# Optimization experiments

Measured on AMD Instinct MI355X. Metric: run time of the kernel, lower is better.

## Reference

```python
import jax, jax.numpy as jnp
import numpy as np


def _cdist(x, y):
    # x: (b, n, c), y: (b, m, c) -> (b, n, m) Euclidean distances
    x2 = jnp.sum(x * x, axis=-1, keepdims=True)          # (b, n, 1)
    y2 = jnp.sum(y * y, axis=-1)[:, None, :]             # (b, 1, m)
    xy = jnp.einsum('bnc,bmc->bnm', x, y)                # (b, n, m)
    d2 = jnp.maximum(x2 + y2 - 2.0 * xy, 0.0)
    return jnp.sqrt(d2)


def setup_inputs() -> dict:
    key = jax.random.key(0)
    k1, k2, k3, k4 = jax.random.split(key, 4)
    bs, N, M, C = 8, 4096, 4096, 128
    return {
        'set1': jax.random.normal(k1, (bs, N, C), dtype=jnp.float32),
        'set2': jax.random.normal(k2, (bs, M, C), dtype=jnp.float32),
        'w1': jax.random.uniform(k3, (bs, N), dtype=jnp.float32),
        'w2': jax.random.uniform(k4, (bs, M), dtype=jnp.float32),
    }


def reference(set1, set2, w1, w2):
    dist = _cdist(set1, set2)                 # (b, N, M)
    out_dist = jnp.min(dist, axis=2)          # (b, N)
    out_dist2 = jnp.min(dist, axis=1)         # (b, M)
    total = (jnp.sum(w1 * out_dist) + jnp.sum(w2 * out_dist2)) / 2.0
    return total
```

## Files before the change

### kernel.cpp

```cpp
#include <hip/hip_runtime.h>

#define BS 8
#define NN 4096
#define MM 4096
#define CC 128
#define XT 128
#define YT 128
#define MH 2048
#define NMT (MH / YT)
#define NXT (NN / XT)

#define FINF_BITS 0x7F800000u

typedef __attribute__((ext_vector_type(8))) short bf16x8;
typedef __attribute__((ext_vector_type(4))) float f32x4;

__device__ inline ushort f2bf(float f) {
    unsigned u = __float_as_uint(f);
    unsigned r = (u + 0x7FFFu + ((u >> 16) & 1u)) >> 16;
    return (ushort)r;
}

__global__ void ch_prep(const float* __restrict__ y,
                        ushort* __restrict__ y16, float* __restrict__ yn,
                        unsigned* __restrict__ rowmin, unsigned* __restrict__ colmin,
                        float* __restrict__ out) {
    int gid = blockIdx.x * blockDim.x + threadIdx.x;
    size_t i = (size_t)gid * 4;

    float4 w = *(const float4*)(y + i);
    ushort4 p;
    p.x = f2bf(w.x); p.y = f2bf(w.y); p.z = f2bf(w.z); p.w = f2bf(w.w);
    *(ushort4*)(y16 + i) = p;
    float sy = w.x * w.x + w.y * w.y + w.z * w.z + w.w * w.w;

#pragma unroll
    for (int mask = 1; mask <= 16; mask <<= 1)
        sy += __shfl_xor(sy, mask, 64);
    if ((threadIdx.x & 31) == 0)
        yn[gid >> 5] = sy;

    if (gid < BS * NN) rowmin[gid] = FINF_BITS;
    if (gid < BS * MM) colmin[gid] = FINF_BITS;
    if (gid == 0) out[0] = 0.0f;
}

__device__ __forceinline__ void stage_y(const ushort* __restrict__ Yb,
                                        ushort* __restrict__ buf,
                                        int tile, int half, int tid, int wave) {
#pragma unroll
    for (int s = 0; s < 4; ++s) {
        int f = s * 256 + tid;
        int r = f >> 3, cslot = f & 7;
        const ushort* g = Yb + (size_t)(tile * YT + r) * CC + half * 64 +
                          ((cslot ^ (r & 7)) * 8);
        ushort* l = buf + (size_t)(s * 256 + wave * 64) * 8;
        __builtin_amdgcn_global_load_lds(
            (const __attribute__((address_space(1))) void*)g,
            (__attribute__((address_space(3))) void*)l, 16, 0, 0);
    }
}

__global__ __launch_bounds__(256) void ch_tile(
    const float* __restrict__ Xf, const ushort* __restrict__ Y,
    const float* __restrict__ yn,
    unsigned* __restrict__ rowmin, unsigned* __restrict__ colmin) {

    __shared__ ushort xs[XT * CC];
    __shared__ ushort ys[2][YT * 64];
    __shared__ unsigned coltile[MH];
    __shared__ unsigned rowtile[XT];
    __shared__ float xnorm[XT];

    const int b  = blockIdx.x;
    const int xt = blockIdx.y;
    const int mh = blockIdx.z;
    const int n0 = xt * XT;
    const int m0 = mh * MH;
    const int tid  = threadIdx.x;
    const int wave = tid >> 6;
    const int lane = tid & 63;
    const int lc   = lane & 15;
    const int quad = lane >> 4;
    const int wm = wave >> 1;
    const int wn = wave & 1;

    const ushort* Yb = Y + ((size_t)b * MM + m0) * CC;

    const float* Xb = Xf + ((size_t)b * NN + n0) * CC;
    {
        float psum[8];
#pragma unroll
        for (int s = 0; s < 8; ++s) {
            int flat = s * 256 + tid;
            int r = flat >> 4, c = flat & 15;
            float4 v0 = *(const float4*)(Xb + (size_t)r * CC + c * 8);
            float4 v1 = *(const float4*)(Xb + (size_t)r * CC + c * 8 + 4);
            ushort h[8] = {f2bf(v0.x), f2bf(v0.y), f2bf(v0.z), f2bf(v0.w),
                           f2bf(v1.x), f2bf(v1.y), f2bf(v1.z), f2bf(v1.w)};
            *(bf16x8*)(xs + r * CC + (c ^ (r & 7)) * 8) = *(bf16x8*)h;
            psum[s] = v0.x * v0.x + v0.y * v0.y + v0.z * v0.z + v0.w * v0.w +
                      v1.x * v1.x + v1.y * v1.y + v1.z * v1.z + v1.w * v1.w;
        }
#pragma unroll
        for (int mask = 1; mask <= 8; mask <<= 1)
#pragma unroll
            for (int s = 0; s < 8; ++s)
                psum[s] += __shfl_xor(psum[s], mask, 64);
        if ((tid & 15) == 0) {
#pragma unroll
            for (int s = 0; s < 8; ++s)
                xnorm[s * 16 + (tid >> 4)] = psum[s];
        }
    }
    for (int c2 = tid; c2 < MH; c2 += 256) coltile[c2] = FINF_BITS;
    if (tid < XT) rowtile[tid] = FINF_BITS;

    stage_y(Yb, ys[0], 0, 0, tid, wave);

    __syncthreads();

    float xnp[4][4];
#pragma unroll
    for (int i = 0; i < 4; ++i) {
        float4 t = *(const float4*)(&xnorm[wm * 64 + i * 16 + quad * 4]);
        xnp[i][0] = t.x; xnp[i][1] = t.y; xnp[i][2] = t.z; xnp[i][3] = t.w;
    }
    float rm[4][4];
#pragma unroll
    for (int i = 0; i < 4; ++i)
#pragma unroll
        for (int r = 0; r < 4; ++r) rm[i][r] = __builtin_inff();

    const float* ynb = yn + (size_t)b * MM + m0;
    const int xrow = (wm * 64 + lc) * CC;
    const int xsw  = lc & 7;

#pragma unroll 1
    for (int t = 0; t < NMT; ++t) {
        float ynr[4];
        f32x4 acc[4][4];
        const f32x4 z = {0.f, 0.f, 0.f, 0.f};

#pragma unroll
        for (int h = 0; h < 2; ++h) {
            const int p = (2 * t + h) & 1;
            if (t + h) __syncthreads();

            const int nh = 2 * t + h + 1;
            if (nh < 2 * NMT)
                stage_y(Yb, ys[p ^ 1], nh >> 1, nh & 1, tid, wave);

            if (h == 0) {
#pragma unroll
                for (int j = 0; j < 4; ++j)
                    ynr[j] = ynb[t * YT + wn * 64 + j * 16 + lc];
            }

            const ushort* yl = ys[p];
#pragma unroll
            for (int s2 = 0; s2 < 2; ++s2) {
                const int ktg = h * 2 + s2;
                bf16x8 af[4], yf[4];
                const int cx = ((ktg * 4 + quad) ^ xsw) * 8;
                const int cy = ((s2 * 4 + quad) ^ xsw) * 8;
#pragma unroll
                for (int j = 0; j < 4; ++j)
                    yf[j] = *(const bf16x8*)(yl + (wn * 64 + j * 16 + lc) * 64 + cy);
#pragma unroll
                for (int i = 0; i < 4; ++i)
                    af[i] = *(const bf16x8*)(xs + xrow + i * 16 * CC + cx);
#pragma unroll
                for (int j = 0; j < 4; ++j)
#pragma unroll
                    for (int i = 0; i < 4; ++i)
                        acc[i][j] = __builtin_amdgcn_mfma_f32_16x16x32_bf16(
                            af[i], yf[j], (ktg == 0) ? z : acc[i][j], 0, 0, 0);
            }
        }

        float cmv[4];
#pragma unroll
        for (int j = 0; j < 4; ++j) cmv[j] = __builtin_inff();

#pragma unroll
        for (int i = 0; i < 4; ++i) {
#pragma unroll
            for (int j = 0; j < 4; ++j) {
                f32x4 a = acc[i][j];
#pragma unroll
                for (int r = 0; r < 4; ++r) {
                    float d2 = xnp[i][r] + fmaf(-2.0f, a[r], ynr[j]);
                    rm[i][r] = fminf(rm[i][r], d2);
                    cmv[j]   = fminf(cmv[j], d2);
                }
            }
        }

#pragma unroll
        for (int mask = 16; mask <= 32; mask <<= 1)
#pragma unroll
            for (int j = 0; j < 4; ++j)
                cmv[j] = fminf(cmv[j], __shfl_xor(cmv[j], mask, 64));
        if (quad == 0) {
#pragma unroll
            for (int j = 0; j < 4; ++j)
                atomicMin(&coltile[t * YT + wn * 64 + j * 16 + lc],
                          __float_as_uint(fmaxf(cmv[j], 0.0f)));
        }
    }

#pragma unroll
    for (int mask = 1; mask <= 8; mask <<= 1)
#pragma unroll
        for (int i = 0; i < 4; ++i)
#pragma unroll
            for (int r = 0; r < 4; ++r)
                rm[i][r] = fminf(rm[i][r], __shfl_xor(rm[i][r], mask, 64));
    if (lc == 0) {
#pragma unroll
        for (int i = 0; i < 4; ++i)
#pragma unroll
            for (int r = 0; r < 4; ++r)
                atomicMin(&rowtile[wm * 64 + i * 16 + quad * 4 + r],
                          __float_as_uint(fmaxf(rm[i][r], 0.0f)));
    }

    __syncthreads();
    if (tid < XT)
        atomicMin(&rowmin[(size_t)b * NN + n0 + tid], rowtile[tid]);
    for (int c2 = tid; c2 < MH; c2 += 256)
        atomicMin(&colmin[(size_t)b * MM + m0 + c2], coltile[c2]);
}

__global__ void ch_finalize(const unsigned* __restrict__ rowmin,
                            const unsigned* __restrict__ colmin,
                            const float* __restrict__ w1,
                            const float* __restrict__ w2,
                            float* __restrict__ out) {
    int i = blockIdx.x * blockDim.x + threadIdx.x;
    int stride = gridDim.x * blockDim.x;
    float s = 0.f;
    for (int idx = i; idx < BS * NN; idx += stride)
        s += w1[idx] * sqrtf(__uint_as_float(rowmin[idx])) +
             w2[idx] * sqrtf(__uint_as_float(colmin[idx]));
#pragma unroll
    for (int off = 32; off > 0; off >>= 1) s += __shfl_down(s, off, 64);
    __shared__ float ls[4];
    int lane = threadIdx.x & 63, wv = threadIdx.x >> 6;
    if (lane == 0) ls[wv] = s;
    __syncthreads();
    if (threadIdx.x == 0) {
        float t = ls[0] + ls[1] + ls[2] + ls[3];
        atomicAdd(out, 0.5f * t);
    }
}

extern "C" void kernel_launch(void* const* d_in, const int* in_sizes, int n_in,
                              void* d_out, int out_size, void* d_ws, size_t ws_size,
                              hipStream_t stream) {
    const float* set1 = (const float*)d_in[0];
    const float* set2 = (const float*)d_in[1];
    const float* w1   = (const float*)d_in[2];
    const float* w2   = (const float*)d_in[3];
    float* out = (float*)d_out;

    ushort*   y16    = (ushort*)d_ws;
    float*    yn     = (float*)(y16 + (size_t)BS * MM * CC);
    unsigned* rowmin = (unsigned*)(yn + BS * MM);
    unsigned* colmin = rowmin + BS * NN;

    ch_prep<<<BS * MM * CC / 4 / 256, 256, 0, stream>>>(
        set2, y16, yn, rowmin, colmin, out);

    dim3 grid(BS, NXT, MM / MH);
    ch_tile<<<grid, 256, 0, stream>>>(set1, y16, yn, rowmin, colmin);

    ch_finalize<<<64, 256, 0, stream>>>(rowmin, colmin, w1, w2, out);
}
```

Measured before the change: 126.3 us.

## Keep X fragments in registers and load Y directly from global with register double-buffering

The LDS-staged Y double buffer, with its per-half-tile block barriers, is replaced. Each wave now loads its Y fragments straight from global memory into registers, ping-ponging between two register sets so the next 64-column tile's loads overlap the current MFMAs. X fragments are loaded from LDS once and held in registers for the whole loop. MFMA issue priority is raised around the matrix ops, and launch bounds request 2 blocks per SM. This removes the barriers and LDS traffic but adds register pressure and uncoalesced global loads, and each wave fetches Y redundantly from global instead of sharing it through LDS.

Result: slower. 147.2 us (+16.6%).

```diff
diff --git a/kernel.cpp b/kernel.cpp
--- a/kernel.cpp
+++ b/kernel.cpp
@@ -5,9 +5,9 @@
 #define MM 4096
 #define CC 128
 #define XT 128
-#define YT 128
 #define MH 2048
-#define NMT (MH / YT)
+#define JT 64
+#define NJ (MH / JT)
 #define NXT (NN / XT)
 
 #define FINF_BITS 0x7F800000u
@@ -45,29 +45,12 @@
     if (gid == 0) out[0] = 0.0f;
 }
 
-__device__ __forceinline__ void stage_y(const ushort* __restrict__ Yb,
-                                        ushort* __restrict__ buf,
-                                        int tile, int half, int tid, int wave) {
-#pragma unroll
-    for (int s = 0; s < 4; ++s) {
-        int f = s * 256 + tid;
-        int r = f >> 3, cslot = f & 7;
-        const ushort* g = Yb + (size_t)(tile * YT + r) * CC + half * 64 +
-                          ((cslot ^ (r & 7)) * 8);
-        ushort* l = buf + (size_t)(s * 256 + wave * 64) * 8;
-        __builtin_amdgcn_global_load_lds(
-            (const __attribute__((address_space(1))) void*)g,
-            (__attribute__((address_space(3))) void*)l, 16, 0, 0);
-    }
-}
-
-__global__ __launch_bounds__(256) void ch_tile(
+__global__ __launch_bounds__(256, 2) void ch_tile(
     const float* __restrict__ Xf, const ushort* __restrict__ Y,
     const float* __restrict__ yn,
     unsigned* __restrict__ rowmin, unsigned* __restrict__ colmin) {
 
     __shared__ ushort xs[XT * CC];
-    __shared__ ushort ys[2][YT * 64];
     __shared__ unsigned coltile[MH];
     __shared__ unsigned rowtile[XT];
     __shared__ float xnorm[XT];
@@ -78,14 +61,15 @@
     const int n0 = xt * XT;
     const int m0 = mh * MH;
     const int tid  = threadIdx.x;
+    const int lane = tid & 63;
     const int wave = tid >> 6;
-    const int lane = tid & 63;
     const int lc   = lane & 15;
     const int quad = lane >> 4;
     const int wm = wave >> 1;
     const int wn = wave & 1;
 
     const ushort* Yb = Y + ((size_t)b * MM + m0) * CC;
+    const float*  ynb = yn + (size_t)b * MM + m0;
 
     const float* Xb = Xf + ((size_t)b * NN + n0) * CC;
     {
@@ -116,9 +100,17 @@
     for (int c2 = tid; c2 < MH; c2 += 256) coltile[c2] = FINF_BITS;
     if (tid < XT) rowtile[tid] = FINF_BITS;
 
-    stage_y(Yb, ys[0], 0, 0, tid, wave);
-
     __syncthreads();
+
+    bf16x8 af[4][4];
+    const int xrow = (wm * 64 + lc) * CC;
+    const int xsw  = lc & 7;
+#pragma unroll
+    for (int kt = 0; kt < 4; ++kt)
+#pragma unroll
+        for (int i = 0; i < 4; ++i)
+            af[kt][i] = *(const bf16x8*)(xs + xrow + i * 16 * CC +
+                                         ((kt * 4 + quad) ^ xsw) * 8);
 
     float xnp[4][4];
 #pragma unroll
@@ -132,82 +124,73 @@
 #pragma unroll
         for (int r = 0; r < 4; ++r) rm[i][r] = __builtin_inff();
 
-    const float* ynb = yn + (size_t)b * MM + m0;
-    const int xrow = (wm * 64 + lc) * CC;
-    const int xsw  = lc & 7;
-
+    auto loadt = [&](bf16x8 (&Yf)[4][2], float (&YN)[2], int j_) {
+        const ushort* py = Yb + (size_t)(j_ * JT + wn * 32 + lc) * CC + quad * 8;
+#pragma unroll
+        for (int jj = 0; jj < 2; ++jj)
+#pragma unroll
+            for (int kt = 0; kt < 4; ++kt)
+                Yf[kt][jj] = *(const bf16x8*)(py + jj * 16 * CC + kt * 32);
+#pragma unroll
+        for (int jj = 0; jj < 2; ++jj)
+            YN[jj] = ynb[j_ * JT + wn * 32 + jj * 16 + lc];
+    };
+
+    auto compt = [&](bf16x8 (&Yf)[4][2], float (&YN)[2], int j_) {
+        f32x4 acc[4][2];
+        const f32x4 z = {0.f, 0.f, 0.f, 0.f};
+#pragma unroll
+        for (int kt = 0; kt < 4; ++kt) {
+            __builtin_amdgcn_s_setprio(1);
+#pragma unroll
+            for (int jj = 0; jj < 2; ++jj)
+#pragma unroll
+                for (int i = 0; i < 4; ++i)
+                    acc[i][jj] = __builtin_amdgcn_mfma_f32_16x16x32_bf16(
+                        af[kt][i], Yf[kt][jj], (kt == 0) ? z : acc[i][jj], 0, 0, 0);
+            __builtin_amdgcn_s_setprio(0);
+        }
+
+        float cmv[2] = {__builtin_inff(), __builtin_inff()};
+#pragma unroll
+        for (int i = 0; i < 4; ++i) {
+            f32x4 a0 = acc[i][0], a1 = acc[i][1];
+            float e0[4], e1[4];
+#pragma unroll
+            for (int r = 0; r < 4; ++r) {
+                e0[r] = xnp[i][r] + fmaf(-2.0f, a0[r], YN[0]);
+                e1[r] = xnp[i][r] + fmaf(-2.0f, a1[r], YN[1]);
+            }
+#pragma unroll
+            for (int r = 0; r < 4; ++r)
+                rm[i][r] = fminf(rm[i][r], fminf(e0[r], e1[r]));
+            cmv[0] = fminf(cmv[0],
+                           fminf(fminf(e0[0], e0[1]), fminf(e0[2], e0[3])));
+            cmv[1] = fminf(cmv[1],
+                           fminf(fminf(e1[0], e1[1]), fminf(e1[2], e1[3])));
+        }
+#pragma unroll
+        for (int mask = 16; mask <= 32; mask <<= 1)
+#pragma unroll
+            for (int jj = 0; jj < 2; ++jj)
+                cmv[jj] = fminf(cmv[jj], __shfl_xor(cmv[jj], mask, 64));
+        if (quad == 0) {
+#pragma unroll
+            for (int jj = 0; jj < 2; ++jj)
+                atomicMin(&coltile[j_ * JT + wn * 32 + jj * 16 + lc],
+                          __float_as_uint(fmaxf(cmv[jj], 0.0f)));
+        }
+    };
+
+    bf16x8 yA[4][2], yB[4][2];
+    float  ynA[2], ynB[2];
+    loadt(yA, ynA, 0);
 #pragma unroll 1
-    for (int t = 0; t < NMT; ++t) {
-        float ynr[4];
-        f32x4 acc[4][4];
-        const f32x4 z = {0.f, 0.f, 0.f, 0.f};
-
-#pragma unroll
-        for (int h = 0; h < 2; ++h) {
-            const int p = (2 * t + h) & 1;
-            if (t + h) __syncthreads();
-
-            const int nh = 2 * t + h + 1;
-            if (nh < 2 * NMT)
-                stage_y(Yb, ys[p ^ 1], nh >> 1, nh & 1, tid, wave);
-
-            if (h == 0) {
-#pragma unroll
-                for (int j = 0; j < 4; ++j)
-                    ynr[j] = ynb[t * YT + wn * 64 + j * 16 + lc];
-            }
-
-            const ushort* yl = ys[p];
-#pragma unroll
-            for (int s2 = 0; s2 < 2; ++s2) {
-                const int ktg = h * 2 + s2;
-                bf16x8 af[4], yf[4];
-                const int cx = ((ktg * 4 + quad) ^ xsw) * 8;
-                const int cy = ((s2 * 4 + quad) ^ xsw) * 8;
-#pragma unroll
-                for (int j = 0; j < 4; ++j)
-                    yf[j] = *(const bf16x8*)(yl + (wn * 64 + j * 16 + lc) * 64 + cy);
-#pragma unroll
-                for (int i = 0; i < 4; ++i)
-                    af[i] = *(const bf16x8*)(xs + xrow + i * 16 * CC + cx);
-#pragma unroll
-                for (int j = 0; j < 4; ++j)
-#pragma unroll
-                    for (int i = 0; i < 4; ++i)
-                        acc[i][j] = __builtin_amdgcn_mfma_f32_16x16x32_bf16(
-                            af[i], yf[j], (ktg == 0) ? z : acc[i][j], 0, 0, 0);
-            }
-        }
-
-        float cmv[4];
-#pragma unroll
-        for (int j = 0; j < 4; ++j) cmv[j] = __builtin_inff();
-
-#pragma unroll
-        for (int i = 0; i < 4; ++i) {
-#pragma unroll
-            for (int j = 0; j < 4; ++j) {
-                f32x4 a = acc[i][j];
-#pragma unroll
-                for (int r = 0; r < 4; ++r) {
-                    float d2 = xnp[i][r] + fmaf(-2.0f, a[r], ynr[j]);
-                    rm[i][r] = fminf(rm[i][r], d2);
-                    cmv[j]   = fminf(cmv[j], d2);
-                }
-            }
-        }
-
-#pragma unroll
-        for (int mask = 16; mask <= 32; mask <<= 1)
-#pragma unroll
-            for (int j = 0; j < 4; ++j)
-                cmv[j] = fminf(cmv[j], __shfl_xor(cmv[j], mask, 64));
-        if (quad == 0) {
-#pragma unroll
-            for (int j = 0; j < 4; ++j)
-                atomicMin(&coltile[t * YT + wn * 64 + j * 16 + lc],
-                          __float_as_uint(fmaxf(cmv[j], 0.0f)));
-        }
+    for (int j = 0; j < NJ; j += 2) {
+        loadt(yB, ynB, j + 1);
+        compt(yA, ynA, j);
+        if (j + 2 < NJ) loadt(yA, ynA, j + 2);
+        compt(yB, ynB, j + 1);
     }
 
 #pragma unroll
```

## Keep X fragments in registers and triple-buffer Y with explicit vmcnt waits

Applied to the files above, without the earlier changes.

The X operand fragments are loaded once into registers, so the X LDS region can be reused as part of a three-slot Y staging buffer. Y tiles are prefetched two stages ahead, with hand-placed s_waitcnt vmcnt and s_barrier replacing __syncthreads, plus s_setprio around the MFMA blocks. The Y norms are preloaded into LDS, launch bounds request two blocks per CU, and the prep kernel handles 8 elements per thread. The aim is to overlap global-to-LDS loads with MFMA work and cut repeated X LDS reads and sync cost. In exchange it raises register pressure and relies on fragile manual waitcnt accounting.

Result: no change. 125.4 us (-0.7%).

```diff
diff --git a/kernel.cpp b/kernel.cpp
--- a/kernel.cpp
+++ b/kernel.cpp
@@ -8,12 +8,17 @@
 #define YT 128
 #define MH 2048
 #define NMT (MH / YT)
+#define NPH (2 * NMT)
 #define NXT (NN / XT)
+#define SLICE (YT * 64)
 
 #define FINF_BITS 0x7F800000u
 
 typedef __attribute__((ext_vector_type(8))) short bf16x8;
 typedef __attribute__((ext_vector_type(4))) float f32x4;
+
+#define WAITVn(n) asm volatile("s_waitcnt vmcnt(" #n ")" ::: "memory")
+#define SCHED_FENCE() __builtin_amdgcn_sched_barrier(0)
 
 __device__ inline ushort f2bf(float f) {
     unsigned u = __float_as_uint(f);
@@ -26,19 +31,21 @@
                         unsigned* __restrict__ rowmin, unsigned* __restrict__ colmin,
                         float* __restrict__ out) {
     int gid = blockIdx.x * blockDim.x + threadIdx.x;
-    size_t i = (size_t)gid * 4;
-
-    float4 w = *(const float4*)(y + i);
-    ushort4 p;
-    p.x = f2bf(w.x); p.y = f2bf(w.y); p.z = f2bf(w.z); p.w = f2bf(w.w);
-    *(ushort4*)(y16 + i) = p;
-    float sy = w.x * w.x + w.y * w.y + w.z * w.z + w.w * w.w;
-
-#pragma unroll
-    for (int mask = 1; mask <= 16; mask <<= 1)
+    size_t i = (size_t)gid * 8;
+
+    float4 w0 = *(const float4*)(y + i);
+    float4 w1 = *(const float4*)(y + i + 4);
+    ushort h[8] = {f2bf(w0.x), f2bf(w0.y), f2bf(w0.z), f2bf(w0.w),
+                   f2bf(w1.x), f2bf(w1.y), f2bf(w1.z), f2bf(w1.w)};
+    *(bf16x8*)(y16 + i) = *(bf16x8*)h;
+    float sy = w0.x * w0.x + w0.y * w0.y + w0.z * w0.z + w0.w * w0.w +
+               w1.x * w1.x + w1.y * w1.y + w1.z * w1.z + w1.w * w1.w;
+
+#pragma unroll
+    for (int mask = 1; mask <= 8; mask <<= 1)
         sy += __shfl_xor(sy, mask, 64);
-    if ((threadIdx.x & 31) == 0)
-        yn[gid >> 5] = sy;
+    if ((threadIdx.x & 15) == 0)
+        yn[gid >> 4] = sy;
 
     if (gid < BS * NN) rowmin[gid] = FINF_BITS;
     if (gid < BS * MM) colmin[gid] = FINF_BITS;
@@ -61,16 +68,16 @@
     }
 }
 
-__global__ __launch_bounds__(256) void ch_tile(
+__global__ __launch_bounds__(256, 2) void ch_tile(
     const float* __restrict__ Xf, const ushort* __restrict__ Y,
     const float* __restrict__ yn,
     unsigned* __restrict__ rowmin, unsigned* __restrict__ colmin) {
 
-    __shared__ ushort xs[XT * CC];
-    __shared__ ushort ys[2][YT * 64];
+    __shared__ ushort pool[3 * SLICE];
     __shared__ unsigned coltile[MH];
     __shared__ unsigned rowtile[XT];
     __shared__ float xnorm[XT];
+    __shared__ float ynld[MH];
 
     const int b  = blockIdx.x;
     const int xt = blockIdx.y;
@@ -78,8 +85,8 @@
     const int n0 = xt * XT;
     const int m0 = mh * MH;
     const int tid  = threadIdx.x;
+    const int lane = tid & 63;
     const int wave = tid >> 6;
-    const int lane = tid & 63;
     const int lc   = lane & 15;
     const int quad = lane >> 4;
     const int wm = wave >> 1;
@@ -87,6 +94,7 @@
 
     const ushort* Yb = Y + ((size_t)b * MM + m0) * CC;
 
+    ushort* xs = pool;
     const float* Xb = Xf + ((size_t)b * NN + n0) * CC;
     {
         float psum[8];
@@ -113,12 +121,26 @@
                 xnorm[s * 16 + (tid >> 4)] = psum[s];
         }
     }
+    {
+        const float* ynb = yn + (size_t)b * MM + m0;
+#pragma unroll
+        for (int s = 0; s < MH / 256; ++s)
+            ynld[s * 256 + tid] = ynb[s * 256 + tid];
+    }
     for (int c2 = tid; c2 < MH; c2 += 256) coltile[c2] = FINF_BITS;
     if (tid < XT) rowtile[tid] = FINF_BITS;
 
-    stage_y(Yb, ys[0], 0, 0, tid, wave);
-
     __syncthreads();
+
+    bf16x8 af[4][4];
+    const int xrow = (wm * 64 + lc) * CC;
+    const int xsw  = lc & 7;
+#pragma unroll
+    for (int kt = 0; kt < 4; ++kt)
+#pragma unroll
+        for (int i = 0; i < 4; ++i)
+            af[kt][i] = *(const bf16x8*)(xs + xrow + i * 16 * CC +
+                                         ((kt * 4 + quad) ^ xsw) * 8);
 
     float xnp[4][4];
 #pragma unroll
@@ -132,81 +154,116 @@
 #pragma unroll
         for (int r = 0; r < 4; ++r) rm[i][r] = __builtin_inff();
 
-    const float* ynb = yn + (size_t)b * MM + m0;
-    const int xrow = (wm * 64 + lc) * CC;
-    const int xsw  = lc & 7;
-
+    __syncthreads();
+
+    stage_y(Yb, pool + 0 * SLICE, 0, 0, tid, wave);
+    stage_y(Yb, pool + 1 * SLICE, 0, 1, tid, wave);
+    WAITVn(4);
+    __builtin_amdgcn_s_barrier();
+    SCHED_FENCE();
+
+    int rd = 0;
 #pragma unroll 1
     for (int t = 0; t < NMT; ++t) {
-        float ynr[4];
         f32x4 acc[4][4];
         const f32x4 z = {0.f, 0.f, 0.f, 0.f};
-
-#pragma unroll
-        for (int h = 0; h < 2; ++h) {
-            const int p = (2 * t + h) & 1;
-            if (t + h) __syncthreads();
-
-            const int nh = 2 * t + h + 1;
-            if (nh < 2 * NMT)
-                stage_y(Yb, ys[p ^ 1], nh >> 1, nh & 1, tid, wave);
-
-            if (h == 0) {
-#pragma unroll
-                for (int j = 0; j < 4; ++j)
-                    ynr[j] = ynb[t * YT + wn * 64 + j * 16 + lc];
-            }
-
-            const ushort* yl = ys[p];
+        float ynr[4];
+
+        {
+            const int ph = 2 * t;
+            const ushort* ybuf = pool + rd * SLICE;
+            if (ph + 2 < NPH) {
+                int wr = rd + 2; if (wr >= 3) wr -= 3;
+                stage_y(Yb, pool + wr * SLICE, (ph + 2) >> 1, (ph + 2) & 1,
+                        tid, wave);
+            }
+#pragma unroll
+            for (int j = 0; j < 4; ++j)
+                ynr[j] = ynld[t * YT + wn * 64 + j * 16 + lc];
 #pragma unroll
             for (int s2 = 0; s2 < 2; ++s2) {
-                const int ktg = h * 2 + s2;
-                bf16x8 af[4], yf[4];
-                const int cx = ((ktg * 4 + quad) ^ xsw) * 8;
+                bf16x8 yf[4];
                 const int cy = ((s2 * 4 + quad) ^ xsw) * 8;
 #pragma unroll
                 for (int j = 0; j < 4; ++j)
-                    yf[j] = *(const bf16x8*)(yl + (wn * 64 + j * 16 + lc) * 64 + cy);
-#pragma unroll
-                for (int i = 0; i < 4; ++i)
-                    af[i] = *(const bf16x8*)(xs + xrow + i * 16 * CC + cx);
+                    yf[j] = *(const bf16x8*)(ybuf + (wn * 64 + j * 16 + lc) * 64 + cy);
+                __builtin_amdgcn_s_setprio(1);
 #pragma unroll
                 for (int j = 0; j < 4; ++j)
 #pragma unroll
                     for (int i = 0; i < 4; ++i)
                         acc[i][j] = __builtin_amdgcn_mfma_f32_16x16x32_bf16(
-                            af[i], yf[j], (ktg == 0) ? z : acc[i][j], 0, 0, 0);
-            }
+                            af[s2][i], yf[j], (s2 == 0) ? z : acc[i][j], 0, 0, 0);
+                __builtin_amdgcn_s_setprio(0);
+            }
+            SCHED_FENCE();
+            if (ph + 2 < NPH) { WAITVn(4); } else { WAITVn(0); }
+            __builtin_amdgcn_s_barrier();
+            SCHED_FENCE();
+            rd = (rd == 2) ? 0 : rd + 1;
         }
 
-        float cmv[4];
-#pragma unroll
-        for (int j = 0; j < 4; ++j) cmv[j] = __builtin_inff();
-
-#pragma unroll
-        for (int i = 0; i < 4; ++i) {
-#pragma unroll
-            for (int j = 0; j < 4; ++j) {
-                f32x4 a = acc[i][j];
-#pragma unroll
-                for (int r = 0; r < 4; ++r) {
-                    float d2 = xnp[i][r] + fmaf(-2.0f, a[r], ynr[j]);
-                    rm[i][r] = fminf(rm[i][r], d2);
-                    cmv[j]   = fminf(cmv[j], d2);
+        {
+            const int ph = 2 * t + 1;
+            const ushort* ybuf = pool + rd * SLICE;
+            if (ph + 2 < NPH) {
+                int wr = rd + 2; if (wr >= 3) wr -= 3;
+                stage_y(Yb, pool + wr * SLICE, (ph + 2) >> 1, (ph + 2) & 1,
+                        tid, wave);
+            }
+#pragma unroll
+            for (int s2 = 0; s2 < 2; ++s2) {
+                bf16x8 yf[4];
+                const int cy = ((s2 * 4 + quad) ^ xsw) * 8;
+#pragma unroll
+                for (int j = 0; j < 4; ++j)
+                    yf[j] = *(const bf16x8*)(ybuf + (wn * 64 + j * 16 + lc) * 64 + cy);
+                __builtin_amdgcn_s_setprio(1);
+#pragma unroll
+                for (int j = 0; j < 4; ++j)
+#pragma unroll
+                    for (int i = 0; i < 4; ++i)
+                        acc[i][j] = __builtin_amdgcn_mfma_f32_16x16x32_bf16(
+                            af[2 + s2][i], yf[j], acc[i][j], 0, 0, 0);
+                __builtin_amdgcn_s_setprio(0);
+            }
+
+            float cmv[4];
+#pragma unroll
+            for (int j = 0; j < 4; ++j) cmv[j] = __builtin_inff();
+#pragma unroll
+            for (int i = 0; i < 4; ++i) {
+#pragma unroll
+                for (int j = 0; j < 4; ++j) {
+                    f32x4 a = acc[i][j];
+                    float e[4];
+#pragma unroll
+                    for (int r = 0; r < 4; ++r)
+                        e[r] = xnp[i][r] + fmaf(-2.0f, a[r], ynr[j]);
+#pragma unroll
+                    for (int r = 0; r < 4; ++r)
+                        rm[i][r] = fminf(rm[i][r], e[r]);
+                    cmv[j] = fminf(cmv[j],
+                                   fminf(fminf(e[0], e[1]), fminf(e[2], e[3])));
                 }
             }
-        }
-
-#pragma unroll
-        for (int mask = 16; mask <= 32; mask <<= 1)
-#pragma unroll
-            for (int j = 0; j < 4; ++j)
-                cmv[j] = fminf(cmv[j], __shfl_xor(cmv[j], mask, 64));
-        if (quad == 0) {
-#pragma unroll
-            for (int j = 0; j < 4; ++j)
-                atomicMin(&coltile[t * YT + wn * 64 + j * 16 + lc],
-                          __float_as_uint(fmaxf(cmv[j], 0.0f)));
+#pragma unroll
+            for (int mask = 16; mask <= 32; mask <<= 1)
+#pragma unroll
+                for (int j = 0; j < 4; ++j)
+                    cmv[j] = fminf(cmv[j], __shfl_xor(cmv[j], mask, 64));
+            if (quad == 0) {
+#pragma unroll
+                for (int j = 0; j < 4; ++j)
+                    atomicMin(&coltile[t * YT + wn * 64 + j * 16 + lc],
+                              __float_as_uint(fmaxf(cmv[j], 0.0f)));
+            }
+
+            SCHED_FENCE();
+            if (ph + 2 < NPH) { WAITVn(4); } else { WAITVn(0); }
+            __builtin_amdgcn_s_barrier();
+            SCHED_FENCE();
+            rd = (rd == 2) ? 0 : rd + 1;
         }
     }
 
@@ -270,7 +327,7 @@
     unsigned* rowmin = (unsigned*)(yn + BS * MM);
     unsigned* colmin = rowmin + BS * NN;
 
-    ch_prep<<<BS * MM * CC / 4 / 256, 256, 0, stream>>>(
+    ch_prep<<<BS * MM * CC / 8 / 256, 256, 0, stream>>>(
         set2, y16, yn, rowmin, colmin, out);
 
     dim3 grid(BS, NXT, MM / MH);
```
